# Performance work log

Measured on AMD Instinct MI355X. Metric: run time of the kernel, lower is better.

Reference implementation:

```python
import jax, jax.numpy as jnp
import numpy as np
from functools import partial

POOL_H, POOL_W = 7, 7


def _bin_index(coord, start, stop, step, n_bins):
    """Map each pixel coordinate to its ROI-pool bin index (or n_bins if outside ROI).

    Bins i < n_bins-1 span [start + i*step, start + (i+1)*step); the last bin
    extends to `stop` (matching the original `(i+1)*h_step if i+1<pool_h else region_h`).
    coord: [L]; start/stop/step: [R] int32. Returns [R, L] int32 in [0, n_bins].
    """
    rel = coord[None, :] - start[:, None]                      # [R, L]
    idx = jnp.minimum(rel // jnp.maximum(step, 1)[:, None], n_bins - 1)
    idx = jnp.where(step[:, None] > 0, idx, n_bins - 1)        # step==0 -> all pixels in last bin
    valid = (rel >= 0) & (coord[None, :] < stop[:, None])
    return jnp.where(valid, idx, n_bins).astype(jnp.int32)


def _roi_pool_image(fm, rois, ph, pw):
    """fm: [H, W, C], rois: [R, 4] relative (h0, w0, h1, w1). Returns [R, ph, pw, C]."""
    H, W, C = fm.shape
    h0 = (H * rois[:, 0]).astype(jnp.int32)   # truncation == tf.cast(..., int32) for >=0
    w0 = (W * rois[:, 1]).astype(jnp.int32)
    h1 = (H * rois[:, 2]).astype(jnp.int32)
    w1 = (W * rois[:, 3]).astype(jnp.int32)
    h_step = (h1 - h0) // ph
    w_step = (w1 - w0) // pw

    idx_h = _bin_index(jnp.arange(H), h0, h1, h_step, ph)      # [R, H]
    idx_w = _bin_index(jnp.arange(W), w0, w1, w_step, pw)      # [R, W]

    neg = jnp.finfo(fm.dtype).min
    fm_whc = jnp.swapaxes(fm, 0, 1)                            # [W, H, C]

    def pool_one(ih, iw):
        # scatter-max columns into width bins (extra slot pw collects out-of-ROI pixels)
        t = jnp.full((pw + 1, H, C), neg, fm.dtype).at[iw].max(fm_whc)[:pw]  # [pw, H, C]
        # scatter-max rows into height bins
        o = jnp.full((ph + 1, pw, C), neg, fm.dtype).at[ih].max(jnp.swapaxes(t, 0, 1))[:ph]
        return o                                               # [ph, pw, C]

    return jax.vmap(pool_one)(idx_h, idx_w)


def setup_inputs() -> dict:
    key = jax.random.key(0)
    k1, k2, k3 = jax.random.split(key, 3)
    feature_map = jax.random.normal(k1, (2, 64, 64, 256), dtype=jnp.float32)
    starts = jax.random.uniform(k2, (2, 256, 2), minval=0.0, maxval=0.3)
    ends = jax.random.uniform(k3, (2, 256, 2), minval=0.6, maxval=1.0)
    rois = jnp.concatenate([starts, ends], axis=-1).astype(jnp.float32)  # (h0, w0, h1, w1)
    return {"feature_map": feature_map, "rois": rois}


def reference(feature_map, rois):
    # per-image ROI max pooling, vmapped over the batch -> [B, R, ph, pw, C]
    pool = partial(_roi_pool_image, ph=POOL_H, pw=POOL_W)
    return jax.vmap(pool)(feature_map, rois)
```

## Files before the change

kernel.cpp:

```cpp
#include <hip/hip_runtime.h>
#include <float.h>

constexpr int H = 64, W = 64, C = 256, PH = 7, PW = 7;

typedef float f32x4 __attribute__((ext_vector_type(4)));

__device__ __forceinline__ f32x4 vmax4(f32x4 a, f32x4 b) {
    f32x4 r;
    r.x = fmaxf(a.x, b.x); r.y = fmaxf(a.y, b.y);
    r.z = fmaxf(a.z, b.z); r.w = fmaxf(a.w, b.w);
    return r;
}

__global__ __launch_bounds__(256) void build_tables(
    const float* __restrict__ fm, float* __restrict__ s4x,
    float* __restrict__ s4y, float* __restrict__ s4xy)
{
    __shared__ f32x4 lds_fm[7][64];
    __shared__ f32x4 lds_sx[7][64];

    const int lane = threadIdx.x & 63;
    const int wave = __builtin_amdgcn_readfirstlane(threadIdx.x >> 6);

    const int b = blockIdx.x & 1;
    const int p = blockIdx.x >> 1;
    const int x = p & (W - 1);
    const int y0 = (p >> 6) << 2;

    const int x1 = min(x + 1, W - 1), x2 = min(x + 2, W - 1), x3 = min(x + 3, W - 1);
    const float* fmb = fm + (size_t)b * H * W * C + (size_t)lane * 4;

    #pragma unroll
    for (int s = 0; s < 2; ++s) {
        const int slot = wave + 4 * s;
        if (slot < 7) {
            const int y = min(y0 + slot, H - 1);
            const float* row = fmb + (size_t)y * W * C;
            f32x4 v0 = *(const f32x4*)(row + (size_t)x  * C);
            f32x4 v1 = *(const f32x4*)(row + (size_t)x1 * C);
            f32x4 v2 = *(const f32x4*)(row + (size_t)x2 * C);
            f32x4 v3 = *(const f32x4*)(row + (size_t)x3 * C);
            lds_fm[slot][lane] = v0;
            lds_sx[slot][lane] = vmax4(vmax4(v0, v1), vmax4(v2, v3));
        }
    }
    __syncthreads();

    const int y = y0 + wave;
    const f32x4 sx = lds_sx[wave][lane];
    const f32x4 sy = vmax4(vmax4(lds_fm[wave][lane],     lds_fm[wave + 1][lane]),
                           vmax4(lds_fm[wave + 2][lane], lds_fm[wave + 3][lane]));
    const f32x4 sxy = vmax4(vmax4(lds_sx[wave][lane],     lds_sx[wave + 1][lane]),
                            vmax4(lds_sx[wave + 2][lane], lds_sx[wave + 3][lane]));

    const size_t o = ((size_t)(b * H + y) * W + x) * C + (size_t)lane * 4;
    *(f32x4*)(s4x  + o) = sx;
    *(f32x4*)(s4y  + o) = sy;
    *(f32x4*)(s4xy + o) = sxy;
}

__global__ __launch_bounds__(256) void roi_pool_q(
    const float* __restrict__ fm, const float* __restrict__ rois,
    const float* __restrict__ s4x, const float* __restrict__ s4y,
    const float* __restrict__ s4xy, float* __restrict__ out, int R)
{
    const int lane = threadIdx.x & 63;
    const int wave = __builtin_amdgcn_readfirstlane(threadIdx.x >> 6);

    const int b = blockIdx.x & 1;
    int m = (blockIdx.x >> 1) * 4 + wave;
    int j = m % PW; m /= PW;
    int i = m % PH; m /= PH;
    int r = m;

    const float* roi = rois + ((size_t)b * R + r) * 4;
    int h0 = (int)((float)H * roi[0]);
    int w0 = (int)((float)W * roi[1]);
    int h1 = (int)((float)H * roi[2]);
    int w1 = (int)((float)W * roi[3]);
    int hs = (h1 - h0) / PH;
    int ws = (w1 - w0) / PW;

    int ys, ye, xs, xe;
    if (hs > 0) { ys = h0 + i * hs; ye = (i < PH - 1) ? (ys + hs) : h1; }
    else        { ys = h0;          ye = (i == PH - 1) ? h1 : h0; }
    if (ws > 0) { xs = w0 + j * ws; xe = (j < PW - 1) ? (xs + ws) : w1; }
    else        { xs = w0;          xe = (j == PW - 1) ? w1 : w0; }
    ys = __builtin_amdgcn_readfirstlane(max(ys, 0));
    ye = __builtin_amdgcn_readfirstlane(min(ye, H));
    xs = __builtin_amdgcn_readfirstlane(max(xs, 0));
    xe = __builtin_amdgcn_readfirstlane(min(xe, W));

    const int hl = ye - ys, wl = xe - xs;
    const f32x4 NEG = {-FLT_MAX, -FLT_MAX, -FLT_MAX, -FLT_MAX};
    f32x4 a0 = NEG, a1 = NEG, a2 = NEG, a3 = NEG;

    if (hl > 0 && wl > 0) {
        const bool y4 = hl >= 4, x4 = wl >= 4;
        const int ny = y4 ? (hl + 3) >> 2 : hl;
        const int nx = x4 ? (wl + 3) >> 2 : wl;
        const int ystep = y4 ? 4 : 1, xstep = x4 ? 4 : 1;
        const int ycl = y4 ? ye - 4 : ye - 1;
        const int xcl = x4 ? xe - 4 : xe - 1;
        const float* tb = y4 ? (x4 ? s4xy : s4y) : (x4 ? s4x : fm);
        const float* tbb = tb + (size_t)b * H * W * C + lane * 4;

        const int xo0 = min(xs,             xcl) * C;
        const int xo1 = min(xs + xstep,     xcl) * C;
        const int xo2 = min(xs + 2 * xstep, xcl) * C;
        const int xo3 = min(xs + 3 * xstep, xcl) * C;

        #pragma unroll
        for (int ky = 0; ky < 4; ++ky) {
            if (ky < ny) {
                const int y = min(ys + ystep * ky, ycl);
                const float* rowp = tbb + (size_t)y * (W * C);
                a0 = vmax4(a0, *(const f32x4*)(rowp + xo0));
                if (nx > 1) a1 = vmax4(a1, *(const f32x4*)(rowp + xo1));
                if (nx > 2) a2 = vmax4(a2, *(const f32x4*)(rowp + xo2));
                if (nx > 3) a3 = vmax4(a3, *(const f32x4*)(rowp + xo3));
            }
        }
    }
    const f32x4 acc = vmax4(vmax4(a0, a1), vmax4(a2, a3));

    size_t o = ((((size_t)b * R + r) * PH + i) * PW + j) * C + (size_t)lane * 4;
    __builtin_nontemporal_store(acc, reinterpret_cast<f32x4*>(out + o));
}

__global__ __launch_bounds__(256) void roi_pool_direct(
    const float* __restrict__ fm, const float* __restrict__ rois,
    float* __restrict__ out, int R)
{
    const int lane = threadIdx.x & 63;
    const int wave = __builtin_amdgcn_readfirstlane(threadIdx.x >> 6);
    const int b = blockIdx.x & 1;
    int m = (blockIdx.x >> 1) * 4 + wave;
    int j = m % PW; m /= PW;
    int i = m % PH; m /= PH;
    int r = m;

    const float* roi = rois + ((size_t)b * R + r) * 4;
    int h0 = (int)((float)H * roi[0]);
    int w0 = (int)((float)W * roi[1]);
    int h1 = (int)((float)H * roi[2]);
    int w1 = (int)((float)W * roi[3]);
    int hs = (h1 - h0) / PH;
    int ws = (w1 - w0) / PW;

    int ys, ye, xs, xe;
    if (hs > 0) { ys = h0 + i * hs; ye = (i < PH - 1) ? (ys + hs) : h1; }
    else        { ys = h0;          ye = (i == PH - 1) ? h1 : h0; }
    if (ws > 0) { xs = w0 + j * ws; xe = (j < PW - 1) ? (xs + ws) : w1; }
    else        { xs = w0;          xe = (j == PW - 1) ? w1 : w0; }
    ys = __builtin_amdgcn_readfirstlane(max(ys, 0));
    ye = __builtin_amdgcn_readfirstlane(min(ye, H));
    xs = __builtin_amdgcn_readfirstlane(max(xs, 0));
    xe = __builtin_amdgcn_readfirstlane(min(xe, W));

    const f32x4 NEG = {-FLT_MAX, -FLT_MAX, -FLT_MAX, -FLT_MAX};
    f32x4 a0 = NEG, a1 = NEG, a2 = NEG, a3 = NEG;
    const float* fmb = fm + (size_t)b * (H * W * C);
    const int lo = lane * 4;

    for (int y = ys; y < ye; y += 2) {
        const int y1 = min(y + 1, ye - 1);
        const int ro0 = y  * (W * C);
        const int ro1 = y1 * (W * C);
        for (int x = xs; x < xe; x += 2) {
            const int x1 = min(x + 1, xe - 1);
            a0 = vmax4(a0, *(const f32x4*)(fmb + ro0 + x  * C + lo));
            a1 = vmax4(a1, *(const f32x4*)(fmb + ro0 + x1 * C + lo));
            a2 = vmax4(a2, *(const f32x4*)(fmb + ro1 + x  * C + lo));
            a3 = vmax4(a3, *(const f32x4*)(fmb + ro1 + x1 * C + lo));
        }
    }
    f32x4 acc = vmax4(vmax4(a0, a1), vmax4(a2, a3));
    size_t o = ((((size_t)b * R + r) * PH + i) * PW + j) * C + (size_t)lo;
    __builtin_nontemporal_store(acc, reinterpret_cast<f32x4*>(out + o));
}

extern "C" void kernel_launch(void* const* d_in, const int* in_sizes, int n_in,
                              void* d_out, int out_size, void* d_ws, size_t ws_size,
                              hipStream_t stream) {
    const float* fm   = (const float*)d_in[0];
    const float* rois = (const float*)d_in[1];
    float* out = (float*)d_out;

    const int B = in_sizes[0] / (H * W * C);
    const int R = in_sizes[1] / (B * 4);

    const size_t tbl = (size_t)B * H * W * C;
    const size_t need = 3 * tbl * sizeof(float);
    const int qblocks = B * (R * PH * PW / 4);

    if (B == 2 && ws_size >= need) {
        float* s4x  = (float*)d_ws;
        float* s4y  = s4x + tbl;
        float* s4xy = s4y + tbl;
        const int bblocks = B * W * (H / 4);
        build_tables<<<bblocks, 256, 0, stream>>>(fm, s4x, s4y, s4xy);
        roi_pool_q  <<<qblocks, 256, 0, stream>>>(fm, rois, s4x, s4y, s4xy, out, R);
    } else {
        roi_pool_direct<<<qblocks, 256, 0, stream>>>(fm, rois, out, R);
    }
}
```

Measured before the change: 27.22 us.

## Stream table build over row ring buffer and batch four bins per wave

build_tables now has each block walk 16 consecutive rows through a 7-slot LDS ring buffer, instead of reloading 7 rows to produce every 4 outputs. That cuts redundant feature-map loads, at the cost of extra barriers and fewer, longer blocks. The s4x and s4y table writes become nontemporal stores. roi_pool_q moves to 512-thread blocks, with each wave computing 4 bins of one ROI (13 wave-groups per ROI), so the ROI decode and setup are shared across bins. The fast path is now restricted to R==256.

Result: slower. 38.78 us (+42.5%).

```diff
diff --git a/kernel.cpp b/kernel.cpp
--- a/kernel.cpp
+++ b/kernel.cpp
@@ -16,8 +16,8 @@
     const float* __restrict__ fm, float* __restrict__ s4x,
     float* __restrict__ s4y, float* __restrict__ s4xy)
 {
-    __shared__ f32x4 lds_fm[7][64];
-    __shared__ f32x4 lds_sx[7][64];
+    __shared__ f32x4 lfm[7][64];
+    __shared__ f32x4 lsx[7][64];
 
     const int lane = threadIdx.x & 63;
     const int wave = __builtin_amdgcn_readfirstlane(threadIdx.x >> 6);
@@ -25,41 +25,47 @@
     const int b = blockIdx.x & 1;
     const int p = blockIdx.x >> 1;
     const int x = p & (W - 1);
-    const int y0 = (p >> 6) << 2;
+    const int k0 = (p >> 6) << 2;
 
     const int x1 = min(x + 1, W - 1), x2 = min(x + 2, W - 1), x3 = min(x + 3, W - 1);
     const float* fmb = fm + (size_t)b * H * W * C + (size_t)lane * 4;
 
-    #pragma unroll
-    for (int s = 0; s < 2; ++s) {
-        const int slot = wave + 4 * s;
-        if (slot < 7) {
-            const int y = min(y0 + slot, H - 1);
-            const float* row = fmb + (size_t)y * W * C;
-            f32x4 v0 = *(const f32x4*)(row + (size_t)x  * C);
-            f32x4 v1 = *(const f32x4*)(row + (size_t)x1 * C);
-            f32x4 v2 = *(const f32x4*)(row + (size_t)x2 * C);
-            f32x4 v3 = *(const f32x4*)(row + (size_t)x3 * C);
-            lds_fm[slot][lane] = v0;
-            lds_sx[slot][lane] = vmax4(vmax4(v0, v1), vmax4(v2, v3));
-        }
-    }
+    auto loadrow = [&](int L) {
+        const int y = min(L, H - 1);
+        const float* row = fmb + (size_t)y * W * C;
+        f32x4 v0 = *(const f32x4*)(row + (size_t)x  * C);
+        f32x4 v1 = *(const f32x4*)(row + (size_t)x1 * C);
+        f32x4 v2 = *(const f32x4*)(row + (size_t)x2 * C);
+        f32x4 v3 = *(const f32x4*)(row + (size_t)x3 * C);
+        lfm[L % 7][lane] = v0;
+        lsx[L % 7][lane] = vmax4(vmax4(v0, v1), vmax4(v2, v3));
+    };
+
+    loadrow(4 * k0 + wave);
+    if (wave < 3) loadrow(4 * k0 + 4 + wave);
     __syncthreads();
 
-    const int y = y0 + wave;
-    const f32x4 sx = lds_sx[wave][lane];
-    const f32x4 sy = vmax4(vmax4(lds_fm[wave][lane],     lds_fm[wave + 1][lane]),
-                           vmax4(lds_fm[wave + 2][lane], lds_fm[wave + 3][lane]));
-    const f32x4 sxy = vmax4(vmax4(lds_sx[wave][lane],     lds_sx[wave + 1][lane]),
-                            vmax4(lds_sx[wave + 2][lane], lds_sx[wave + 3][lane]));
-
-    const size_t o = ((size_t)(b * H + y) * W + x) * C + (size_t)lane * 4;
-    *(f32x4*)(s4x  + o) = sx;
-    *(f32x4*)(s4y  + o) = sy;
-    *(f32x4*)(s4xy + o) = sxy;
-}
-
-__global__ __launch_bounds__(256) void roi_pool_q(
+    for (int k = k0; ; ++k) {
+        const int y = 4 * k + wave;
+        const f32x4 sx  = lsx[y % 7][lane];
+        const f32x4 sy  = vmax4(vmax4(lfm[y % 7][lane], lfm[(y + 1) % 7][lane]),
+                                vmax4(lfm[(y + 2) % 7][lane], lfm[(y + 3) % 7][lane]));
+        const f32x4 sxy = vmax4(vmax4(lsx[y % 7][lane], lsx[(y + 1) % 7][lane]),
+                                vmax4(lsx[(y + 2) % 7][lane], lsx[(y + 3) % 7][lane]));
+
+        const size_t o = ((size_t)(b * H + y) * W + x) * C + (size_t)lane * 4;
+        __builtin_nontemporal_store(sx, reinterpret_cast<f32x4*>(s4x + o));
+        __builtin_nontemporal_store(sy, reinterpret_cast<f32x4*>(s4y + o));
+        *(f32x4*)(s4xy + o) = sxy;
+
+        if (k == k0 + 3) break;
+        __syncthreads();
+        loadrow(4 * (k + 1) + 3 + wave);
+        __syncthreads();
+    }
+}
+
+__global__ __launch_bounds__(512) void roi_pool_q(
     const float* __restrict__ fm, const float* __restrict__ rois,
     const float* __restrict__ s4x, const float* __restrict__ s4y,
     const float* __restrict__ s4xy, float* __restrict__ out, int R)
@@ -68,64 +74,80 @@
     const int wave = __builtin_amdgcn_readfirstlane(threadIdx.x >> 6);
 
     const int b = blockIdx.x & 1;
-    int m = (blockIdx.x >> 1) * 4 + wave;
-    int j = m % PW; m /= PW;
-    int i = m % PH; m /= PH;
-    int r = m;
-
-    const float* roi = rois + ((size_t)b * R + r) * 4;
-    int h0 = (int)((float)H * roi[0]);
-    int w0 = (int)((float)W * roi[1]);
-    int h1 = (int)((float)H * roi[2]);
-    int w1 = (int)((float)W * roi[3]);
-    int hs = (h1 - h0) / PH;
-    int ws = (w1 - w0) / PW;
-
-    int ys, ye, xs, xe;
-    if (hs > 0) { ys = h0 + i * hs; ye = (i < PH - 1) ? (ys + hs) : h1; }
-    else        { ys = h0;          ye = (i == PH - 1) ? h1 : h0; }
-    if (ws > 0) { xs = w0 + j * ws; xe = (j < PW - 1) ? (xs + ws) : w1; }
-    else        { xs = w0;          xe = (j == PW - 1) ? w1 : w0; }
-    ys = __builtin_amdgcn_readfirstlane(max(ys, 0));
-    ye = __builtin_amdgcn_readfirstlane(min(ye, H));
-    xs = __builtin_amdgcn_readfirstlane(max(xs, 0));
-    xe = __builtin_amdgcn_readfirstlane(min(xe, W));
-
-    const int hl = ye - ys, wl = xe - xs;
-    const f32x4 NEG = {-FLT_MAX, -FLT_MAX, -FLT_MAX, -FLT_MAX};
-    f32x4 a0 = NEG, a1 = NEG, a2 = NEG, a3 = NEG;
-
-    if (hl > 0 && wl > 0) {
-        const bool y4 = hl >= 4, x4 = wl >= 4;
-        const int ny = y4 ? (hl + 3) >> 2 : hl;
-        const int nx = x4 ? (wl + 3) >> 2 : wl;
-        const int ystep = y4 ? 4 : 1, xstep = x4 ? 4 : 1;
-        const int ycl = y4 ? ye - 4 : ye - 1;
-        const int xcl = x4 ? xe - 4 : xe - 1;
-        const float* tb = y4 ? (x4 ? s4xy : s4y) : (x4 ? s4x : fm);
-        const float* tbb = tb + (size_t)b * H * W * C + lane * 4;
-
-        const int xo0 = min(xs,             xcl) * C;
-        const int xo1 = min(xs + xstep,     xcl) * C;
-        const int xo2 = min(xs + 2 * xstep, xcl) * C;
-        const int xo3 = min(xs + 3 * xstep, xcl) * C;
-
-        #pragma unroll
-        for (int ky = 0; ky < 4; ++ky) {
-            if (ky < ny) {
-                const int y = min(ys + ystep * ky, ycl);
-                const float* rowp = tbb + (size_t)y * (W * C);
-                a0 = vmax4(a0, *(const f32x4*)(rowp + xo0));
-                if (nx > 1) a1 = vmax4(a1, *(const f32x4*)(rowp + xo1));
-                if (nx > 2) a2 = vmax4(a2, *(const f32x4*)(rowp + xo2));
-                if (nx > 3) a3 = vmax4(a3, *(const f32x4*)(rowp + xo3));
+    const int q = blockIdx.x >> 1;
+    const int gw = q * 8 + wave;
+    const int r  = gw / 13;
+    const int c  = gw - 13 * r;
+
+    const f32x4 rv = *(const f32x4*)(rois + ((size_t)b * R + r) * 4);
+    int h0 = (int)((float)H * rv.x);
+    int w0 = (int)((float)W * rv.y);
+    int h1 = (int)((float)H * rv.z);
+    int w1 = (int)((float)W * rv.w);
+    h0 = __builtin_amdgcn_readfirstlane(h0);
+    w0 = __builtin_amdgcn_readfirstlane(w0);
+    h1 = __builtin_amdgcn_readfirstlane(h1);
+    w1 = __builtin_amdgcn_readfirstlane(w1);
+    const int hs = (h1 - h0) / PH;
+    const int ws = (w1 - w0) / PW;
+
+    const size_t img = (size_t)b * H * W * C;
+    const float* fmb   = fm   + img + lane * 4;
+    const float* s4xb  = s4x  + img + lane * 4;
+    const float* s4yb  = s4y  + img + lane * 4;
+    const float* s4xyb = s4xy + img + lane * 4;
+    const size_t obase = (((size_t)b * R + r) * PH * PW) * C + (size_t)lane * 4;
+
+    #pragma unroll
+    for (int t = 0; t < 4; ++t) {
+        const int id = min(c * 4 + t, PH * PW - 1);
+        const int i = id / PW;
+        const int j = id - PW * i;
+
+        int ys, ye, xs, xe;
+        if (hs > 0) { ys = h0 + i * hs; ye = (i < PH - 1) ? (ys + hs) : h1; }
+        else        { ys = h0;          ye = (i == PH - 1) ? h1 : h0; }
+        if (ws > 0) { xs = w0 + j * ws; xe = (j < PW - 1) ? (xs + ws) : w1; }
+        else        { xs = w0;          xe = (j == PW - 1) ? w1 : w0; }
+        ys = __builtin_amdgcn_readfirstlane(max(ys, 0));
+        ye = __builtin_amdgcn_readfirstlane(min(ye, H));
+        xs = __builtin_amdgcn_readfirstlane(max(xs, 0));
+        xe = __builtin_amdgcn_readfirstlane(min(xe, W));
+
+        const int hl = ye - ys, wl = xe - xs;
+        const f32x4 NEG = {-FLT_MAX, -FLT_MAX, -FLT_MAX, -FLT_MAX};
+        f32x4 a0 = NEG, a1 = NEG, a2 = NEG, a3 = NEG;
+
+        if (hl > 0 && wl > 0) {
+            const bool y4 = hl >= 4, x4 = wl >= 4;
+            const int ny = y4 ? (hl + 3) >> 2 : hl;
+            const int nx = x4 ? (wl + 3) >> 2 : wl;
+            const int ystep = y4 ? 4 : 1, xstep = x4 ? 4 : 1;
+            const int ycl = y4 ? ye - 4 : ye - 1;
+            const int xcl = x4 ? xe - 4 : xe - 1;
+            const float* tbb = y4 ? (x4 ? s4xyb : s4yb) : (x4 ? s4xb : fmb);
+
+            const int xo0 = min(xs,             xcl) * C;
+            const int xo1 = min(xs + xstep,     xcl) * C;
+            const int xo2 = min(xs + 2 * xstep, xcl) * C;
+            const int xo3 = min(xs + 3 * xstep, xcl) * C;
+
+            #pragma unroll
+            for (int ky = 0; ky < 4; ++ky) {
+                if (ky < ny) {
+                    const int y = min(ys + ystep * ky, ycl);
+                    const float* rowp = tbb + (size_t)y * (W * C);
+                    a0 = vmax4(a0, *(const f32x4*)(rowp + xo0));
+                    if (nx > 1) a1 = vmax4(a1, *(const f32x4*)(rowp + xo1));
+                    if (nx > 2) a2 = vmax4(a2, *(const f32x4*)(rowp + xo2));
+                    if (nx > 3) a3 = vmax4(a3, *(const f32x4*)(rowp + xo3));
+                }
             }
         }
-    }
-    const f32x4 acc = vmax4(vmax4(a0, a1), vmax4(a2, a3));
-
-    size_t o = ((((size_t)b * R + r) * PH + i) * PW + j) * C + (size_t)lane * 4;
-    __builtin_nontemporal_store(acc, reinterpret_cast<f32x4*>(out + o));
+        const f32x4 acc = vmax4(vmax4(a0, a1), vmax4(a2, a3));
+        __builtin_nontemporal_store(acc,
+            reinterpret_cast<f32x4*>(out + obase + (size_t)id * C));
+    }
 }
 
 __global__ __launch_bounds__(256) void roi_pool_direct(
@@ -192,16 +214,17 @@
 
     const size_t tbl = (size_t)B * H * W * C;
     const size_t need = 3 * tbl * sizeof(float);
-    const int qblocks = B * (R * PH * PW / 4);
-
-    if (B == 2 && ws_size >= need) {
+
+    if (B == 2 && R == 256 && ws_size >= need) {
         float* s4x  = (float*)d_ws;
         float* s4y  = s4x + tbl;
         float* s4xy = s4y + tbl;
-        const int bblocks = B * W * (H / 4);
+        const int bblocks = B * W * 4;
+        const int qblocks = B * (R * 13 / 8) * 2 / 2;
         build_tables<<<bblocks, 256, 0, stream>>>(fm, s4x, s4y, s4xy);
-        roi_pool_q  <<<qblocks, 256, 0, stream>>>(fm, rois, s4x, s4y, s4xy, out, R);
+        roi_pool_q  <<<qblocks, 512, 0, stream>>>(fm, rois, s4x, s4y, s4xy, out, R);
     } else {
+        const int qblocks = B * (R * PH * PW / 4);
         roi_pool_direct<<<qblocks, 256, 0, stream>>>(fm, rois, out, R);
     }
 }
```
